# Optimization experiments

Hardware: AMD Instinct MI355X
Metric: run time of the kernel (lower is better)

Reference implementation:

```python
import jax, jax.numpy as jnp
import numpy as np

GRID = 52
NUM_BOXES = 2
NUM_CLASSES = 5
LAMBDA_COORD = 5.0
LAMBDA_CONF = 1.0
LAMBDA_CLASS = 1.0
ALPHA = 0.25
GAMMA = 2.0
CH = NUM_BOXES * (5 + NUM_CLASSES)  # 20
B = 256


def setup_inputs() -> dict:
    key = jax.random.key(0)
    k1, k2 = jax.random.split(key)
    predictions = jax.random.normal(k1, (B, GRID, GRID, CH), dtype=jnp.float32)
    targets = jax.random.uniform(k2, (B, GRID, GRID, CH), dtype=jnp.float32)
    return {"predictions": predictions, "targets": targets}


def _focal_elementwise(logits, t):
    # stable BCE-with-logits, elementwise
    ce = jnp.maximum(logits, 0.0) - logits * t + jnp.log1p(jnp.exp(-jnp.abs(logits)))
    p = jax.nn.sigmoid(logits)
    p_t = p * t + (1.0 - p) * (1.0 - t)
    alpha_t = ALPHA * t + (1.0 - ALPHA) * (1.0 - t)
    return alpha_t * (1.0 - p_t) ** GAMMA * ce


def reference(predictions, targets):
    nb5 = NUM_BOXES * 5
    # [B, S, S, num_boxes, 5]
    pred_box = predictions[..., :nb5].reshape(B, GRID, GRID, NUM_BOXES, 5)
    tgt_box = targets[..., :nb5].reshape(B, GRID, GRID, NUM_BOXES, 5)

    pred_conf = pred_box[..., 4]  # [B,S,S,NB]
    tgt_conf = tgt_box[..., 4]
    has_obj = (tgt_conf > 0.5).astype(predictions.dtype)  # [B,S,S,NB]
    num_objects = jnp.maximum(jnp.sum(has_obj), 1.0)

    # confidence: per-scalar focal (reduction='mean' on a single element == element)
    conf_loss = jnp.sum(_focal_elementwise(pred_conf, tgt_conf)) / B

    # coordinates: masked sum of squared errors over x,y,w,h
    sq = jnp.sum((pred_box[..., :4] - tgt_box[..., :4]) ** 2, axis=-1)  # [B,S,S,NB]
    coord_loss = jnp.sum(has_obj * sq) / B

    # classification: CE per cell, counted once per object box in that cell
    pred_cls = predictions[..., nb5:nb5 + NUM_CLASSES]  # [B,S,S,C]
    tgt_idx = jnp.argmax(targets[..., nb5:nb5 + NUM_CLASSES], axis=-1)  # [B,S,S]
    logp = jax.nn.log_softmax(pred_cls, axis=-1)
    nll = -jnp.take_along_axis(logp, tgt_idx[..., None], axis=-1)[..., 0]  # [B,S,S]
    obj_count = jnp.sum(has_obj, axis=-1)  # [B,S,S] number of object boxes per cell
    class_loss = jnp.sum(obj_count * nll) / num_objects

    total_loss = LAMBDA_COORD * coord_loss + LAMBDA_CONF * conf_loss + LAMBDA_CLASS * class_loss
    return total_loss
```

## Files before the change

### kernel.cpp

```cpp
#include <hip/hip_runtime.h>


constexpr int   kB        = 256;
constexpr int   kGrid     = 52;
constexpr int   kCells    = kB * kGrid * kGrid;
constexpr int   kBlocks   = kCells / 256;
constexpr float kAlpha    = 0.25f;
constexpr float kLamCoord = 5.0f;

constexpr int kStride = 17;

__device__ __forceinline__ void stage_and_read(const float4* __restrict__ src4,
                                               int base4, int tid,
                                               float* lds, float (&out)[16])
{
    const float4 r0 = src4[base4 + tid];
    const float4 r1 = src4[base4 + 256  + tid];
    const float4 r2 = src4[base4 + 512  + tid];
    const float4 r3 = src4[base4 + 768  + tid];
    const float4 r4 = src4[base4 + 1024 + tid];

    #pragma unroll
    for (int k = 0; k < 5; ++k) {
        const int f    = k * 256 + tid;
        const int cell = f / 5;
        const int rem  = f - cell * 5;
        if (rem != 4) {
            const float4 v = (k == 0) ? r0 : (k == 1) ? r1 : (k == 2) ? r2
                           : (k == 3) ? r3 : r4;
            const int a = cell * kStride + rem * 4;
            lds[a + 0] = v.x; lds[a + 1] = v.y;
            lds[a + 2] = v.z; lds[a + 3] = v.w;
        }
    }
    __syncthreads();

    #pragma unroll
    for (int j = 0; j < 16; ++j) out[j] = lds[tid * kStride + j];
}

__global__ __launch_bounds__(256) void phobia_main_kernel(
    const float4* __restrict__ pred4,
    const float4* __restrict__ tgt4,
    float4* __restrict__ part)
{
    __shared__ float lds[256 * kStride];
    __shared__ float sred[4][4];

    const int tid   = threadIdx.x;
    const int base4 = blockIdx.x * 1280;

    float p[16], t[16];
    stage_and_read(pred4, base4, tid, lds, p);
    __syncthreads();
    stage_and_read(tgt4, base4, tid, lds, t);

    float coord = 0.f, conf = 0.f, cls = 0.f;

    float obj_count = 0.f;
    #pragma unroll
    for (int n = 0; n < 2; ++n) {
        const int b5    = n * 5;
        const float l   = p[b5 + 4];
        const float tc  = t[b5 + 4];
        const float has = (tc > 0.5f) ? 1.f : 0.f;

        float sq = 0.f;
        #pragma unroll
        for (int k = 0; k < 4; ++k) {
            const float d = p[b5 + k] - t[b5 + k];
            sq += d * d;
        }
        coord += has * sq;

        const float ce = fmaxf(l, 0.f) - l * tc + log1pf(__expf(-fabsf(l)));
        const float s  = 1.f / (1.f + __expf(-l));
        const float pt = s * tc + (1.f - s) * (1.f - tc);
        const float at = kAlpha * tc + (1.f - kAlpha) * (1.f - tc);
        const float om = 1.f - pt;
        conf += at * om * om * ce;

        obj_count += has;
    }

    float bv = t[10], pv = p[10];
    if (t[11] > bv) { bv = t[11]; pv = p[11]; }
    if (t[12] > bv) { bv = t[12]; pv = p[12]; }
    if (t[13] > bv) { bv = t[13]; pv = p[13]; }
    if (t[14] > bv) { bv = t[14]; pv = p[14]; }

    const float m  = fmaxf(fmaxf(fmaxf(p[10], p[11]), fmaxf(p[12], p[13])), p[14]);
    const float se = __expf(p[10] - m) + __expf(p[11] - m) + __expf(p[12] - m)
                   + __expf(p[13] - m) + __expf(p[14] - m);
    cls = obj_count * (__logf(se) + m - pv);

    float nobj = obj_count;

    #pragma unroll
    for (int off = 32; off >= 1; off >>= 1) {
        coord += __shfl_down(coord, off);
        conf  += __shfl_down(conf,  off);
        cls   += __shfl_down(cls,   off);
        nobj  += __shfl_down(nobj,  off);
    }

    const int wave = tid >> 6;
    const int lane = tid & 63;
    if (lane == 0) {
        sred[wave][0] = coord; sred[wave][1] = conf;
        sred[wave][2] = cls;   sred[wave][3] = nobj;
    }
    __syncthreads();
    if (tid == 0) {
        float4 o;
        o.x = sred[0][0] + sred[1][0] + sred[2][0] + sred[3][0];
        o.y = sred[0][1] + sred[1][1] + sred[2][1] + sred[3][1];
        o.z = sred[0][2] + sred[1][2] + sred[2][2] + sred[3][2];
        o.w = sred[0][3] + sred[1][3] + sred[2][3] + sred[3][3];
        part[blockIdx.x] = o;
    }
}

__global__ __launch_bounds__(256) void phobia_reduce_kernel(
    const float4* __restrict__ part, float* __restrict__ out)
{
    const int tid = threadIdx.x;
    float c0 = 0.f, c1 = 0.f, c2 = 0.f, c3 = 0.f;
    for (int i = tid; i < kBlocks; i += 256) {
        const float4 v = part[i];
        c0 += v.x; c1 += v.y; c2 += v.z; c3 += v.w;
    }
    #pragma unroll
    for (int off = 32; off >= 1; off >>= 1) {
        c0 += __shfl_down(c0, off);
        c1 += __shfl_down(c1, off);
        c2 += __shfl_down(c2, off);
        c3 += __shfl_down(c3, off);
    }
    __shared__ float sred[4][4];
    const int wave = tid >> 6;
    const int lane = tid & 63;
    if (lane == 0) {
        sred[wave][0] = c0; sred[wave][1] = c1;
        sred[wave][2] = c2; sred[wave][3] = c3;
    }
    __syncthreads();
    if (tid == 0) {
        const float coord = sred[0][0] + sred[1][0] + sred[2][0] + sred[3][0];
        const float conf  = sred[0][1] + sred[1][1] + sred[2][1] + sred[3][1];
        const float cls   = sred[0][2] + sred[1][2] + sred[2][2] + sred[3][2];
        const float nobj  = sred[0][3] + sred[1][3] + sred[2][3] + sred[3][3];
        out[0] = kLamCoord * (coord / (float)kB)
               + (conf / (float)kB)
               + cls / fmaxf(nobj, 1.f);
    }
}

extern "C" void kernel_launch(void* const* d_in, const int* in_sizes, int n_in,
                              void* d_out, int out_size, void* d_ws, size_t ws_size,
                              hipStream_t stream) {
    const float4* pred4 = (const float4*)d_in[0];
    const float4* tgt4  = (const float4*)d_in[1];
    float4* part = (float4*)d_ws;
    float* out = (float*)d_out;

    phobia_main_kernel<<<kBlocks, 256, 0, stream>>>(pred4, tgt4, part);
    phobia_reduce_kernel<<<1, 256, 0, stream>>>(part, out);
}
```

Measured before the change: 28.36 us.

## Stage inputs via direct global-to-LDS async loads instead of register staging

Replaces the register-based load and scatter into a padded LDS tile with __builtin_amdgcn_global_load_lds, which copies both prediction and target tiles straight into contiguous LDS. Both tiles are loaded together before a single barrier, and each thread then reads its cell's first four float4s from LDS. This removes the VGPR round trip, the divide-by-5 address math and one barrier, and overlaps the two input loads. In exchange it uses more LDS (40KB per block), which may reduce occupancy, and the unpadded float4 reads at a stride of five float4s may cause LDS bank conflicts.

```diff
diff --git a/kernel.cpp b/kernel.cpp
--- a/kernel.cpp
+++ b/kernel.cpp
@@ -8,55 +8,43 @@
 constexpr float kAlpha    = 0.25f;
 constexpr float kLamCoord = 5.0f;
 
-constexpr int kStride = 17;
-
-__device__ __forceinline__ void stage_and_read(const float4* __restrict__ src4,
-                                               int base4, int tid,
-                                               float* lds, float (&out)[16])
-{
-    const float4 r0 = src4[base4 + tid];
-    const float4 r1 = src4[base4 + 256  + tid];
-    const float4 r2 = src4[base4 + 512  + tid];
-    const float4 r3 = src4[base4 + 768  + tid];
-    const float4 r4 = src4[base4 + 1024 + tid];
-
-    #pragma unroll
-    for (int k = 0; k < 5; ++k) {
-        const int f    = k * 256 + tid;
-        const int cell = f / 5;
-        const int rem  = f - cell * 5;
-        if (rem != 4) {
-            const float4 v = (k == 0) ? r0 : (k == 1) ? r1 : (k == 2) ? r2
-                           : (k == 3) ? r3 : r4;
-            const int a = cell * kStride + rem * 4;
-            lds[a + 0] = v.x; lds[a + 1] = v.y;
-            lds[a + 2] = v.z; lds[a + 3] = v.w;
-        }
-    }
-    __syncthreads();
-
-    #pragma unroll
-    for (int j = 0; j < 16; ++j) out[j] = lds[tid * kStride + j];
-}
+#define AS1(p) ((const __attribute__((address_space(1))) void*)(p))
+#define AS3(p) ((__attribute__((address_space(3))) void*)(p))
 
 __global__ __launch_bounds__(256) void phobia_main_kernel(
     const float4* __restrict__ pred4,
     const float4* __restrict__ tgt4,
     float4* __restrict__ part)
 {
-    __shared__ float lds[256 * kStride];
-    __shared__ float sred[4][4];
+    __shared__ float4 ldsP[1280];
+    __shared__ float4 ldsT[1280];
+    __shared__ float  sred[4][4];
 
-    const int tid   = threadIdx.x;
-    const int base4 = blockIdx.x * 1280;
+    const int tid  = threadIdx.x;
+    const int wave = tid >> 6;
+    const int lane = tid & 63;
+    const size_t base4 = (size_t)blockIdx.x * 1280;
 
-    float p[16], t[16];
-    stage_and_read(pred4, base4, tid, lds, p);
+    #pragma unroll
+    for (int k = 0; k < 5; ++k) {
+        const int f  = k * 256 + tid;
+        const int fw = k * 256 + wave * 64;
+        __builtin_amdgcn_global_load_lds(AS1(pred4 + base4 + f), AS3(ldsP + fw), 16, 0, 0);
+        __builtin_amdgcn_global_load_lds(AS1(tgt4  + base4 + f), AS3(ldsT + fw), 16, 0, 0);
+    }
     __syncthreads();
-    stage_and_read(tgt4, base4, tid, lds, t);
 
-    float coord = 0.f, conf = 0.f, cls = 0.f;
+    const float4 P0 = ldsP[tid * 5 + 0], P1 = ldsP[tid * 5 + 1];
+    const float4 P2 = ldsP[tid * 5 + 2], P3 = ldsP[tid * 5 + 3];
+    const float4 T0 = ldsT[tid * 5 + 0], T1 = ldsT[tid * 5 + 1];
+    const float4 T2 = ldsT[tid * 5 + 2], T3 = ldsT[tid * 5 + 3];
 
+    const float p[16] = {P0.x, P0.y, P0.z, P0.w,  P1.x, P1.y, P1.z, P1.w,
+                         P2.x, P2.y, P2.z, P2.w,  P3.x, P3.y, P3.z, P3.w};
+    const float t[16] = {T0.x, T0.y, T0.z, T0.w,  T1.x, T1.y, T1.z, T1.w,
+                         T2.x, T2.y, T2.z, T2.w,  T3.x, T3.y, T3.z, T3.w};
+
+    float coord = 0.f, conf = 0.f;
     float obj_count = 0.f;
     #pragma unroll
     for (int n = 0; n < 2; ++n) {
@@ -92,8 +80,9 @@
     const float m  = fmaxf(fmaxf(fmaxf(p[10], p[11]), fmaxf(p[12], p[13])), p[14]);
     const float se = __expf(p[10] - m) + __expf(p[11] - m) + __expf(p[12] - m)
                    + __expf(p[13] - m) + __expf(p[14] - m);
-    cls = obj_count * (__logf(se) + m - pv);
+    const float cls0 = obj_count * (__logf(se) + m - pv);
 
+    float cls  = cls0;
     float nobj = obj_count;
 
     #pragma unroll
@@ -104,8 +93,6 @@
         nobj  += __shfl_down(nobj,  off);
     }
 
-    const int wave = tid >> 6;
-    const int lane = tid & 63;
     if (lane == 0) {
         sred[wave][0] = coord; sred[wave][1] = conf;
         sred[wave][2] = cls;   sred[wave][3] = nobj;
```

Result: faster. 27.28 us (-3.8%).
